# Optimization experiments

Hardware: AMD Instinct MI355X
Metric: run time of the kernel (lower is better)

The kernel has to match this reference:

```python
import jax, jax.numpy as jnp
import numpy as np

EMBED_DIM = 1024
NUM_HEADS = 8
HEAD_DIM = EMBED_DIM // NUM_HEADS  # 128
MAX_DIST = 128
RADIUS = 256
R = 2 * MAX_DIST + 1  # 257 relative-position embeddings


def setup_inputs() -> dict:
    key = jax.random.key(0)
    ks = jax.random.split(key, 8)
    B, Sq, Sk = 4, 1024, 1024
    s = 0.02
    return {
        "Q": jax.random.normal(ks[0], (B, Sq, EMBED_DIM), jnp.float32),
        "K": jax.random.normal(ks[1], (B, Sk, EMBED_DIM), jnp.float32),
        "V": jax.random.normal(ks[2], (B, Sk, EMBED_DIM), jnp.float32),
        "segment_ids": jnp.zeros((B, Sq), jnp.int32),
        "key_padding_mask": jnp.zeros((B, Sk), jnp.bool_),
        "Wq": jax.random.normal(ks[3], (EMBED_DIM, EMBED_DIM), jnp.float32) * s,
        "Wk": jax.random.normal(ks[4], (EMBED_DIM, EMBED_DIM), jnp.float32) * s,
        "Wv": jax.random.normal(ks[5], (EMBED_DIM, EMBED_DIM), jnp.float32) * s,
        "Wo": jax.random.normal(ks[6], (EMBED_DIM, EMBED_DIM), jnp.float32) * s,
        "rel_emb": jax.random.normal(ks[7], (NUM_HEADS, R, HEAD_DIM), jnp.float32) * s,
    }


def _proj(x, W, B, S):
    # Linear (no bias) then split heads: (B,S,d) -> (B*h, S, head_dim)
    y = x @ W.T
    return y.reshape(B, S, NUM_HEADS, HEAD_DIM).transpose(0, 2, 1, 3).reshape(B * NUM_HEADS, S, HEAD_DIM)


def _attention(Q, K, V, key_padding_mask, Wq, Wk, Wv, Wo, rel_emb):
    B, Sq, _ = Q.shape
    Sk = K.shape[1]
    Qp = _proj(Q, Wq, B, Sq)
    Kp = _proj(K, Wk, B, Sk)
    Vp = _proj(V, Wv, B, Sk)

    iq = jnp.arange(Sq)
    ik = jnp.arange(Sk)
    # clipped relative offsets -> bias table indices, shape (Sq, Sk)
    rel_ids = jnp.clip(ik[None, :] - iq[:, None], -MAX_DIST, MAX_DIST) + MAX_DIST

    # per-head table tiled over batch: (B*h, R, head_dim)
    rel_embeds = jnp.broadcast_to(rel_emb[None], (B, NUM_HEADS, R, HEAD_DIM)).reshape(B * NUM_HEADS, R, HEAD_DIM)

    Q_rel = jnp.einsum('bqd,brd->bqr', Qp, rel_embeds)        # (B*h, Sq, R)
    energy = jnp.einsum('bqd,bkd->bqk', Qp, Kp)               # (B*h, Sq, Sk)
    rel_shift = Q_rel[:, iq[:, None], rel_ids]                # gather along R -> (B*h, Sq, Sk)
    energy = (energy + rel_shift) / jnp.sqrt(jnp.float32(HEAD_DIM))

    local_mask = jnp.abs(ik[None, :] - iq[:, None]) > RADIUS  # (Sq, Sk) slided band
    mask = local_mask[None, None] | key_padding_mask[:, None, None, :]  # (B,1,Sq,Sk)
    mask = jnp.broadcast_to(mask, (B, NUM_HEADS, Sq, Sk)).reshape(B * NUM_HEADS, Sq, Sk)
    energy = jnp.where(mask, -jnp.inf, energy)

    attn = jax.nn.softmax(energy, axis=2)
    out = jnp.matmul(attn, Vp)                                # (B*h, Sq, head_dim)
    # permute(0,2,3,1): head_dim-major then head, matching the torch module
    out = out.reshape(B, NUM_HEADS, Sq, HEAD_DIM).transpose(0, 2, 3, 1).reshape(B, Sq, HEAD_DIM * NUM_HEADS)
    return out @ Wo.T


def reference(Q, K, V, segment_ids, key_padding_mask, Wq, Wk, Wv, Wo, rel_emb):
    # segment_ids is unused by the 'slided' RPE variant
    return _attention(Q, K, V, key_padding_mask, Wq, Wk, Wv, Wo, rel_emb)
```

## Files before the change

### kernel.cpp

```cpp
#include <hip/hip_runtime.h>

typedef __attribute__((ext_vector_type(8))) short short8;
typedef __attribute__((ext_vector_type(4))) short short4v;
typedef __attribute__((ext_vector_type(4))) float float4a;
typedef __attribute__((ext_vector_type(16))) float float16a;
typedef __attribute__((ext_vector_type(4))) unsigned int uint4v;

#define MFMA16(a, b, c) __builtin_amdgcn_mfma_f32_16x16x32_bf16(a, b, c, 0, 0, 0)
#define MFMA32(a, b, c) __builtin_amdgcn_mfma_f32_32x32x16_bf16(a, b, c, 0, 0, 0)

static __device__ __forceinline__ short f2bf(float f) {
  unsigned u = __builtin_bit_cast(unsigned, f);
  u += 0x7fff + ((u >> 16) & 1);
  return (short)(u >> 16);
}
static __device__ __forceinline__ float bf2f(short s) {
  unsigned u = ((unsigned)(unsigned short)s) << 16;
  return __builtin_bit_cast(float, u);
}

static __device__ __forceinline__ void gl2lds(const short* g, short* l) {
  __builtin_amdgcn_global_load_lds(
      (const __attribute__((address_space(1))) void*)g,
      (__attribute__((address_space(3))) void*)l,
      16, 0, 0);
}

struct Cvt8 { const float* in[8]; short* out[8]; };
__global__ __launch_bounds__(256) void cvt8_k(Cvt8 a) {
  int b = blockIdx.x, seg, rb;
  if (b < 12288)      { seg = b >> 12;                 rb = b & 4095; }
  else if (b < 16384) { seg = 3 + ((b - 12288) >> 10); rb = (b - 12288) & 1023; }
  else                { seg = 7;                       rb = b - 16384; }
  int i = rb * 256 + threadIdx.x;
  if (seg == 6) {
    int o = i * 4;
    int n = o >> 10, kp = o & 1023;
    int h = kp >> 7, d0 = kp & 127;
    const float* src = a.in[6] + n * 1024 + h;
    short4v s;
    s.x = f2bf(src[d0 * 8]);
    s.y = f2bf(src[d0 * 8 + 8]);
    s.z = f2bf(src[d0 * 8 + 16]);
    s.w = f2bf(src[d0 * 8 + 24]);
    ((short4v*)a.out[6])[i] = s;
    return;
  }
  float4a v = ((const float4a*)a.in[seg])[i];
  short4v o;
  o.x = f2bf(v.x); o.y = f2bf(v.y); o.z = f2bf(v.z); o.w = f2bf(v.w);
  ((short4v*)a.out[seg])[i] = o;
}

__global__ __launch_bounds__(256) void gemm_qkv(
    const short* __restrict__ Qb, const short* __restrict__ Kb, const short* __restrict__ Vb,
    const short* __restrict__ Wq, const short* __restrict__ Wk, const short* __restrict__ Wv,
    short* __restrict__ Qp, short* __restrict__ Kp, short* __restrict__ Vt) {
  __shared__ short pool[32768];
  int bid = blockIdx.x;
  int xcd = bid & 7, slot = bid >> 3;
  int seg = slot >> 5, r = slot & 31;
  int mt = ((xcd >> 1) << 3) | (r >> 2);
  int nt = ((xcd & 1) << 2) | (r & 3);
  const short* A = seg == 0 ? Qb : (seg == 1 ? Kb : Vb);
  const short* W = seg == 0 ? Wq : (seg == 1 ? Wk : Wv);
  int m0 = mt * 128, n0 = nt * 128;
  int tid = threadIdx.x;
  int lane = tid & 63, wid = tid >> 6;
  int l15 = lane & 15, quad = lane >> 4;
  int wm = wid & 1, wn = wid >> 1;

  int srow = lane >> 3, sunit = (lane & 7) ^ (lane >> 3);
  const short* gA = A + (m0 + wid * 32 + srow) * 1024 + sunit * 8;
  const short* gB = W + (n0 + wid * 32 + srow) * 1024 + sunit * 8;
  int stoff = (wid * 32) * 64;
  int sw = l15 & 7;

  float4a acc[4][4];
#pragma unroll
  for (int i = 0; i < 4; ++i)
#pragma unroll
    for (int j = 0; j < 4; ++j) acc[i][j] = (float4a){0, 0, 0, 0};

#pragma unroll
  for (int t = 0; t < 4; ++t) {
    gl2lds(gA + t * 8192, pool + stoff + t * 512);
    gl2lds(gB + t * 8192, pool + 8192 + stoff + t * 512);
  }
  __syncthreads();

  int cur = 0;
  for (int kc = 0; kc < 1024; kc += 64) {
    if (kc < 960) {
      short* nxt = pool + ((cur ^ 1) << 14);
#pragma unroll
      for (int t = 0; t < 4; ++t) {
        gl2lds(gA + kc + 64 + t * 8192, nxt + stoff + t * 512);
        gl2lds(gB + kc + 64 + t * 8192, nxt + 8192 + stoff + t * 512);
      }
    }
    const short* As = pool + (cur << 14);
    const short* Bs = As + 8192;
#pragma unroll
    for (int ks = 0; ks < 2; ++ks) {
      short8 af[4], bfr[4];
#pragma unroll
      for (int i = 0; i < 4; ++i)
        af[i] = *(const short8*)&As[(wm * 64 + i * 16 + l15) * 64 +
                                    (((ks * 4 + quad) ^ sw) * 8)];
#pragma unroll
      for (int j = 0; j < 4; ++j)
        bfr[j] = *(const short8*)&Bs[(wn * 64 + j * 16 + l15) * 64 +
                                     (((ks * 4 + quad) ^ sw) * 8)];
#pragma unroll
      for (int i = 0; i < 4; ++i)
#pragma unroll
        for (int j = 0; j < 4; ++j) acc[i][j] = MFMA16(af[i], bfr[j], acc[i][j]);
    }
    __syncthreads();
    cur ^= 1;
  }

  if (seg < 2) {
    float scl = (seg == 0) ? 0.12752745707470575f : 1.0f;
#pragma unroll
    for (int i = 0; i < 4; ++i)
#pragma unroll
      for (int j = 0; j < 4; ++j)
#pragma unroll
        for (int r2 = 0; r2 < 4; ++r2) {
          int m = m0 + wm * 64 + i * 16 + quad * 4 + r2;
          int n = n0 + wn * 64 + j * 16 + l15;
          int bb = m >> 10, s = m & 1023, hh = n >> 7, d = n & 127;
          short v = f2bf(acc[i][j][r2] * scl);
          if (seg == 0) Qp[(((bb * 8 + hh) * 1024) + s) * 128 + d] = v;
          else          Kp[(((bb * 8 + hh) * 1024) + s) * 128 + d] = v;
        }
  } else {
    short* T = pool;
    int b2 = m0 >> 10, s0 = m0 & 1023;
    long vb2 = (long)(b2 * 8 + nt) * 131072;
#pragma unroll
    for (int hd = 0; hd < 2; ++hd) {
      __syncthreads();
      if (wn == hd) {
#pragma unroll
        for (int j = 0; j < 4; ++j)
#pragma unroll
          for (int i = 0; i < 4; ++i)
#pragma unroll
            for (int r2 = 0; r2 < 4; ++r2)
              T[(j * 16 + l15) * 132 + wm * 64 + i * 16 + quad * 4 + r2] =
                  f2bf(acc[i][j][r2]);
      }
      __syncthreads();
#pragma unroll
      for (int rr = 0; rr < 4; ++rr) {
        int d = rr * 16 + (tid >> 4);
        short8 v = *(const short8*)&T[d * 132 + (tid & 15) * 8];
        *(short8*)&Vt[vb2 + (hd * 64 + d) * 1024 + s0 + (tid & 15) * 8] = v;
      }
    }
  }
}

__global__ __launch_bounds__(256) void gemm_o(const short* __restrict__ A,
                                              const short* __restrict__ W,
                                              float* __restrict__ C) {
  __shared__ short pool[24576];
  int bid = blockIdx.x;
  int xcd = bid & 7, slot = bid >> 3;
  int mt = ((xcd >> 1) << 3) | (slot >> 3);
  int nt = ((xcd & 1) << 3) | (slot & 7);
  int m0 = mt * 128, n0 = nt * 64;
  int lane = threadIdx.x & 63, wid = threadIdx.x >> 6;
  int l15 = lane & 15, quad = lane >> 4;
  int wm = wid & 1, wn = wid >> 1;

  int srow = lane >> 3, sunit = (lane & 7) ^ (lane >> 3);
  int bb = m0 >> 10, q0t = m0 & 1023;
  const short* gA = A + bb * 1048576 + (q0t + wid * 32 + srow) * 128 + sunit * 8;
  const short* gB = W + (n0 + wid * 16 + srow) * 1024 + sunit * 8;
  int saoff = (wid * 32) * 64;
  int sboff = (wid * 16) * 64;
  int sw = l15 & 7;

  float4a acc[4][2];
#pragma unroll
  for (int i = 0; i < 4; ++i)
#pragma unroll
    for (int j = 0; j < 2; ++j) acc[i][j] = (float4a){0, 0, 0, 0};

#pragma unroll
  for (int t = 0; t < 4; ++t) gl2lds(gA + t * 1024, pool + saoff + t * 512);
#pragma unroll
  for (int t = 0; t < 2; ++t) gl2lds(gB + t * 8192, pool + 8192 + sboff + t * 512);
  __syncthreads();

  int cur = 0;
  for (int kc = 0; kc < 1024; kc += 64) {
    if (kc < 960) {
      int kn = kc + 64;
      int koff = (kn >> 7) * 131072 + (kn & 64);
      short* nxt = pool + ((cur ^ 1) * 12288);
#pragma unroll
      for (int t = 0; t < 4; ++t) gl2lds(gA + koff + t * 1024, nxt + saoff + t * 512);
#pragma unroll
      for (int t = 0; t < 2; ++t) gl2lds(gB + kn + t * 8192, nxt + 8192 + sboff + t * 512);
    }
    const short* As = pool + cur * 12288;
    const short* Bs = As + 8192;
#pragma unroll
    for (int ks = 0; ks < 2; ++ks) {
      short8 af[4], bfr[2];
#pragma unroll
      for (int i = 0; i < 4; ++i)
        af[i] = *(const short8*)&As[(wm * 64 + i * 16 + l15) * 64 +
                                    (((ks * 4 + quad) ^ sw) * 8)];
#pragma unroll
      for (int j = 0; j < 2; ++j)
        bfr[j] = *(const short8*)&Bs[(wn * 32 + j * 16 + l15) * 64 +
                                     (((ks * 4 + quad) ^ sw) * 8)];
#pragma unroll
      for (int i = 0; i < 4; ++i)
#pragma unroll
        for (int j = 0; j < 2; ++j) acc[i][j] = MFMA16(af[i], bfr[j], acc[i][j]);
    }
    __syncthreads();
    cur ^= 1;
  }

#pragma unroll
  for (int i = 0; i < 4; ++i)
#pragma unroll
    for (int j = 0; j < 2; ++j)
#pragma unroll
      for (int r2 = 0; r2 < 4; ++r2) {
        int m = m0 + wm * 64 + i * 16 + quad * 4 + r2;
        int n = n0 + wn * 32 + j * 16 + l15;
        C[m * 1024 + n] = acc[i][j][r2];
      }
}

__global__ __launch_bounds__(256) void qrel_k(const short* __restrict__ Qp,
                                              const short* __restrict__ rel,
                                              short* __restrict__ Qrel) {
  int lane = threadIdx.x & 63, wid = threadIdx.x >> 6;
  int gw = blockIdx.x * 4 + wid;
  int bh = gw / 1088;
  int rem = gw - bh * 1088;
  int mt = rem / 17;
  int nt = rem - mt * 17;
  int l15 = lane & 15, quad = lane >> 4;
  int h = bh & 7;

  const short* arow = Qp + bh * 131072 + (mt * 16 + l15) * 128 + quad * 8;
  int col = nt * 16 + l15;
  int colc = col > 256 ? 256 : col;
  const short* brow = rel + (h * 257 + colc) * 128 + quad * 8;

  float4a acc = {0, 0, 0, 0};
#pragma unroll
  for (int kc = 0; kc < 128; kc += 32) {
    short8 a = *(const short8*)(arow + kc);
    short8 b = *(const short8*)(brow + kc);
    acc = MFMA16(a, b, acc);
  }
  if (col < 257) {
#pragma unroll
    for (int r = 0; r < 4; ++r) {
      int q = mt * 16 + quad * 4 + r;
      Qrel[bh * 264192 + q * 258 + col] = f2bf(acc[r]);
    }
  }
}

__global__ __launch_bounds__(256, 2) void attn_k(const short* __restrict__ Qp,
                                                 const short* __restrict__ Kp,
                                                 const short* __restrict__ Vt,
                                                 const short* __restrict__ Qrel,
                                                 const unsigned char* __restrict__ kpm,
                                                 short* __restrict__ O2) {
  __shared__ __align__(16) short pool[16512];
  short* qlds = pool;
  float* obuf = (float*)pool;
  float* lbuf = (float*)pool + 8192;
  int tid = threadIdx.x;
  int lane = tid & 63, wid = tid >> 6;
  int qt = wid & 1, half = wid >> 1;
  int bid = blockIdx.x;
  int bh = ((bid & 7) << 2) | ((bid >> 3) & 3);
  int qsb = bid >> 5;
  int Q0 = qsb * 64;
  int q0 = Q0 + qt * 32;
  int l31 = lane & 31, hl = lane >> 5;
  int b = bh >> 3;

  {
    const short8* src = (const short8*)(Qrel + bh * 264192 + Q0 * 258);
    short8* dst = (short8*)qlds;
    for (int i = tid; i < 2064; i += 256) dst[i] = src[i];
  }

  short8 aq[8];
  const short* qrow = Qp + bh * 131072 + (q0 + l31) * 128 + hl * 8;
#pragma unroll
  for (int s = 0; s < 8; ++s) aq[s] = *(const short8*)(qrow + s * 16);
  __syncthreads();

  float16a O[4];
#pragma unroll
  for (int d = 0; d < 4; ++d)
#pragma unroll
    for (int i = 0; i < 16; ++i) O[d][i] = 0.f;
  float lsum = 0.f;

  int klo = Q0 - 256; if (klo < 0) klo = 0;
  int khi = Q0 + 320; if (khi > 1024) khi = 1024;

  const short* kbase = Kp + bh * 131072 + hl * 8;
  const short* vbase = Vt + bh * 131072 + hl * 8;
  const unsigned char* pmrow = kpm + b * 1024;
  int qv = q0 + l31;
  int rowb = (qt * 32 + l31) * 258;

  int k0 = klo + half * 32;
  short8 kb[8];
  unsigned pm32 = 0;
  {
    const short* krow = kbase + (k0 + l31) * 128;
#pragma unroll
    for (int s = 0; s < 8; ++s) kb[s] = *(const short8*)(krow + s * 16);
    pm32 = (unsigned)__ballot(pmrow[k0 + l31] != 0);
  }

  for (; k0 < khi; k0 += 64) {
    unsigned pmc = pm32;
    float16a S;
#pragma unroll
    for (int i = 0; i < 16; ++i) S[i] = 0.f;
#pragma unroll
    for (int s = 0; s < 8; ++s) S = MFMA32(kb[s], aq[s], S);

    int kn = k0 + 64;
    unsigned char pmb = 0;
    if (kn < khi) {
      const short* krow = kbase + (kn + l31) * 128;
#pragma unroll
      for (int s = 0; s < 8; ++s) kb[s] = *(const short8*)(krow + s * 16);
      pmb = pmrow[kn + l31];
    }

    short8 vb0[4], vb1[4];
#pragma unroll
    for (int dblk = 0; dblk < 4; ++dblk) {
      const short* vrow = vbase + (dblk * 32 + l31) * 1024 + k0;
      vb0[dblk] = *(const short8*)(vrow);
      vb1[dblk] = *(const short8*)(vrow + 16);
    }

    int dq = k0 - qv;
    bool edge = (k0 - q0 < -224) | (k0 - q0 > 224) | (pmc != 0);
    if (!edge) {
      int rb = dq + 4 * hl + 128;
#pragma unroll
      for (int i = 0; i < 16; ++i) {
        int rr = rb + (i & 3) + 8 * (i >> 2);
        rr = rr < 0 ? 0 : (rr > 256 ? 256 : rr);
        float pe = __builtin_amdgcn_exp2f(S[i] + bf2f(qlds[rowb + rr]));
        S[i] = pe;
        lsum += pe;
      }
    } else {
#pragma unroll
      for (int i = 0; i < 16; ++i) {
        int koff = (i & 3) + 8 * (i >> 2) + 4 * hl;
        int dd = dq + koff;
        int rr = dd < -128 ? 0 : (dd > 128 ? 256 : dd + 128);
        float rel = bf2f(qlds[rowb + rr]);
        int msk = (dd < -256) | (dd > 256) | (int)((pmc >> koff) & 1u);
        float pe = msk ? 0.f : __builtin_amdgcn_exp2f(S[i] + rel);
        S[i] = pe;
        lsum += pe;
      }
    }

    short8 ap0, ap1;
    {
      unsigned x0, y0, z0, w0;
      asm("v_cvt_pk_bf16_f32 %0, %1, %2" : "=v"(x0) : "v"(S[0]), "v"(S[1]));
      asm("v_cvt_pk_bf16_f32 %0, %1, %2" : "=v"(y0) : "v"(S[2]), "v"(S[3]));
      asm("v_cvt_pk_bf16_f32 %0, %1, %2" : "=v"(z0) : "v"(S[4]), "v"(S[5]));
      asm("v_cvt_pk_bf16_f32 %0, %1, %2" : "=v"(w0) : "v"(S[6]), "v"(S[7]));
      asm("v_permlane32_swap_b32 %0, %1" : "+v"(x0), "+v"(z0));
      asm("v_permlane32_swap_b32 %0, %1" : "+v"(y0), "+v"(w0));
      uint4v u0 = {x0, y0, z0, w0};
      ap0 = __builtin_bit_cast(short8, u0);
      unsigned x1, y1, z1, w1;
      asm("v_cvt_pk_bf16_f32 %0, %1, %2" : "=v"(x1) : "v"(S[8]), "v"(S[9]));
      asm("v_cvt_pk_bf16_f32 %0, %1, %2" : "=v"(y1) : "v"(S[10]), "v"(S[11]));
      asm("v_cvt_pk_bf16_f32 %0, %1, %2" : "=v"(z1) : "v"(S[12]), "v"(S[13]));
      asm("v_cvt_pk_bf16_f32 %0, %1, %2" : "=v"(w1) : "v"(S[14]), "v"(S[15]));
      asm("v_permlane32_swap_b32 %0, %1" : "+v"(x1), "+v"(z1));
      asm("v_permlane32_swap_b32 %0, %1" : "+v"(y1), "+v"(w1));
      uint4v u1 = {x1, y1, z1, w1};
      ap1 = __builtin_bit_cast(short8, u1);
    }

#pragma unroll
    for (int dblk = 0; dblk < 4; ++dblk) {
      O[dblk] = MFMA32(ap0, vb0[dblk], O[dblk]);
      O[dblk] = MFMA32(ap1, vb1[dblk], O[dblk]);
    }

    pm32 = (unsigned)__ballot(pmb != 0);
  }

  lsum += __shfl_xor(lsum, 32);
  __syncthreads();
  if (half == 1) {
    if (hl == 0) lbuf[qt * 32 + l31] = lsum;
#pragma unroll
    for (int dblk = 0; dblk < 4; ++dblk)
#pragma unroll
      for (int i = 0; i < 16; ++i) {
        int qoff = (i & 3) + 8 * (i >> 2) + 4 * hl;
        obuf[(qt * 32 + qoff) * 128 + dblk * 32 + l31] = O[dblk][i];
      }
  }
  __syncthreads();
  if (half == 0) {
    if (hl == 0) {
      float inv = __builtin_amdgcn_rcpf(lsum + lbuf[qt * 32 + l31]);
      lbuf[qt * 32 + l31] = inv;
    }
#pragma unroll
    for (int dblk = 0; dblk < 4; ++dblk)
#pragma unroll
      for (int i = 0; i < 16; ++i) {
        int qoff = (i & 3) + 8 * (i >> 2) + 4 * hl;
        obuf[(qt * 32 + qoff) * 128 + dblk * 32 + l31] += O[dblk][i];
      }
  }
  __syncthreads();

#pragma unroll
  for (int it = 0; it < 4; ++it) {
    int idx = tid + it * 256;
    int q = idx >> 4, d = (idx & 15) * 8;
    float inv = lbuf[q];
    const float* ob = &obuf[q * 128 + d];
    short8 v;
#pragma unroll
    for (int j = 0; j < 8; ++j) v[j] = f2bf(ob[j] * inv);
    *(short8*)&O2[(long)bh * 131072 + (long)(Q0 + q) * 128 + d] = v;
  }
}

extern "C" void kernel_launch(void* const* d_in, const int* in_sizes, int n_in,
                              void* d_out, int out_size, void* d_ws, size_t ws_size,
                              hipStream_t stream) {
  const float* Q   = (const float*)d_in[0];
  const float* K   = (const float*)d_in[1];
  const float* V   = (const float*)d_in[2];
  const unsigned char* kpm = (const unsigned char*)d_in[4];
  const float* Wq  = (const float*)d_in[5];
  const float* Wk  = (const float*)d_in[6];
  const float* Wv  = (const float*)d_in[7];
  const float* Wo  = (const float*)d_in[8];
  const float* rel = (const float*)d_in[9];
  float* out = (float*)d_out;

  short* ws = (short*)d_ws;
  short* Qb   = ws;
  short* Kb   = Qb + 4194304;
  short* Vb   = Kb + 4194304;
  short* Wqb  = Vb + 4194304;
  short* Wkb  = Wqb + 1048576;
  short* Wvb  = Wkb + 1048576;
  short* Wob  = Wvb + 1048576;
  short* relb = Wob + 1048576;
  short* Qp   = relb + 263168;
  short* Kp   = Qp + 4194304;
  short* Vt   = Kp + 4194304;
  short* O2   = Vt + 4194304;
  short* Qrel = Qb;

  Cvt8 ca;
  ca.in[0] = Q;  ca.out[0] = Qb;
  ca.in[1] = K;  ca.out[1] = Kb;
  ca.in[2] = V;  ca.out[2] = Vb;
  ca.in[3] = Wq; ca.out[3] = Wqb;
  ca.in[4] = Wk; ca.out[4] = Wkb;
  ca.in[5] = Wv; ca.out[5] = Wvb;
  ca.in[6] = Wo; ca.out[6] = Wob;
  ca.in[7] = rel; ca.out[7] = relb;
  cvt8_k<<<dim3(16641), dim3(256), 0, stream>>>(ca);

  gemm_qkv<<<dim3(768), dim3(256), 0, stream>>>(Qb, Kb, Vb, Wqb, Wkb, Wvb, Qp, Kp, Vt);
  qrel_k<<<dim3(8704), dim3(256), 0, stream>>>(Qp, relb, Qrel);
  attn_k<<<dim3(512), dim3(256), 0, stream>>>(Qp, Kp, Vt, Qrel, kpm, O2);
  gemm_o<<<dim3(512), dim3(256), 0, stream>>>(O2, Wob, out);
}
```

Measured before the change: 239.7 us.

## Stage K/V tiles through LDS with async global_load_lds and swizzled layout

Replaces per-wave direct global loads of K and V fragments with cooperative block-level staging into shared memory via global_load_lds, using XOR-swizzled layouts to avoid bank conflicts. Each 64-key tile is loaded once per block and shared by both query-tile waves, which removes the duplicate global traffic between the two waves that previously read the same keys. The cost is doubled LDS allocation, which may reduce occupancy, and two block-wide barriers per iteration. The prefetch of the next tile is issued after the first barrier and overlaps the current tile's compute.

```diff
diff --git a/kernel.cpp b/kernel.cpp
--- a/kernel.cpp
+++ b/kernel.cpp
@@ -281,13 +281,15 @@
                                                  const short* __restrict__ Qrel,
                                                  const unsigned char* __restrict__ kpm,
                                                  short* __restrict__ O2) {
-  __shared__ __align__(16) short pool[16512];
+  __shared__ __align__(16) short pool[32896];
   short* qlds = pool;
-  float* obuf = (float*)pool;
-  float* lbuf = (float*)pool + 8192;
+  short* Kbuf = pool + 16512;
+  short* Vbuf = pool + 16512 + 8192;
+  float* obuf = (float*)(pool + 16512);
+  float* lbuf = (float*)pool;
   int tid = threadIdx.x;
   int lane = tid & 63, wid = tid >> 6;
-  int qt = wid & 1, half = wid >> 1;
+  int qt = wid & 1, kh = wid >> 1;
   int bid = blockIdx.x;
   int bh = ((bid & 7) << 2) | ((bid >> 3) & 3);
   int qsb = bid >> 5;
@@ -296,17 +298,46 @@
   int l31 = lane & 31, hl = lane >> 5;
   int b = bh >> 3;
 
+  int klo = Q0 - 256; if (klo < 0) klo = 0;
+  int khi = Q0 + 320; if (khi > 1024) khi = 1024;
+
+  const short* kgbase = Kp + (long)bh * 131072;
+  const short* vgbase = Vt + (long)bh * 131072;
+  const unsigned char* pmrow = kpm + b * 1024;
+
+  int ksr = lane >> 4, ksu = lane & 15;
+  int vsr = lane >> 3, vsu = (lane & 7) ^ (lane >> 3);
+
+#define STAGE_KV(KT)                                                          \
+  {                                                                           \
+    int _k0 = (KT);                                                           \
+    _Pragma("unroll")                                                         \
+    for (int c = 0; c < 4; ++c) {                                             \
+      int rl = wid * 16 + c * 4 + ksr;                                        \
+      gl2lds(kgbase + (long)(_k0 + rl) * 128 + ((ksu ^ (c * 4 + ksr)) * 8),   \
+             Kbuf + (wid * 16 + c * 4) * 128);                                \
+    }                                                                         \
+    _Pragma("unroll")                                                         \
+    for (int c = 0; c < 4; ++c) {                                             \
+      int rl = wid * 32 + c * 8 + vsr;                                        \
+      gl2lds(vgbase + (long)rl * 1024 + _k0 + vsu * 8,                        \
+             Vbuf + (wid * 32 + c * 8) * 64);                                 \
+    }                                                                         \
+  }
+
   {
     const short8* src = (const short8*)(Qrel + bh * 264192 + Q0 * 258);
     short8* dst = (short8*)qlds;
     for (int i = tid; i < 2064; i += 256) dst[i] = src[i];
   }
-
   short8 aq[8];
   const short* qrow = Qp + bh * 131072 + (q0 + l31) * 128 + hl * 8;
 #pragma unroll
   for (int s = 0; s < 8; ++s) aq[s] = *(const short8*)(qrow + s * 16);
+  STAGE_KV(klo);
+  unsigned char pmb = pmrow[klo + kh * 32 + l31];
   __syncthreads();
+  unsigned pm32 = (unsigned)__ballot(pmb != 0);
 
   float16a O[4];
 #pragma unroll
@@ -315,52 +346,43 @@
     for (int i = 0; i < 16; ++i) O[d][i] = 0.f;
   float lsum = 0.f;
 
-  int klo = Q0 - 256; if (klo < 0) klo = 0;
-  int khi = Q0 + 320; if (khi > 1024) khi = 1024;
-
-  const short* kbase = Kp + bh * 131072 + hl * 8;
-  const short* vbase = Vt + bh * 131072 + hl * 8;
-  const unsigned char* pmrow = kpm + b * 1024;
   int qv = q0 + l31;
   int rowb = (qt * 32 + l31) * 258;
-
-  int k0 = klo + half * 32;
-  short8 kb[8];
-  unsigned pm32 = 0;
-  {
-    const short* krow = kbase + (k0 + l31) * 128;
-#pragma unroll
-    for (int s = 0; s < 8; ++s) kb[s] = *(const short8*)(krow + s * 16);
-    pm32 = (unsigned)__ballot(pmrow[k0 + l31] != 0);
-  }
-
-  for (; k0 < khi; k0 += 64) {
+  int r15 = l31 & 15;
+  int d7 = l31 & 7;
+
+  for (int k0 = klo; k0 < khi; k0 += 64) {
+    int kw = k0 + kh * 32;
+    short8 kf[8];
+    const short* Kr = Kbuf + (kh * 32 + l31) * 128;
+#pragma unroll
+    for (int s = 0; s < 8; ++s)
+      kf[s] = *(const short8*)&Kr[(((2 * s + hl) ^ r15) * 8)];
+    short8 vf0[4], vf1[4];
+#pragma unroll
+    for (int dblk = 0; dblk < 4; ++dblk) {
+      const short* Vr = Vbuf + (dblk * 32 + l31) * 64;
+      vf0[dblk] = *(const short8*)&Vr[(((kh * 4 + hl) ^ d7) * 8)];
+      vf1[dblk] = *(const short8*)&Vr[(((kh * 4 + 2 + hl) ^ d7) * 8)];
+    }
+    __syncthreads();
+
+    int k1 = k0 + 64;
+    unsigned char pmn = 0;
+    if (k1 < khi) {
+      STAGE_KV(k1);
+      pmn = pmrow[k1 + kh * 32 + l31];
+    }
     unsigned pmc = pm32;
+
     float16a S;
 #pragma unroll
     for (int i = 0; i < 16; ++i) S[i] = 0.f;
 #pragma unroll
-    for (int s = 0; s < 8; ++s) S = MFMA32(kb[s], aq[s], S);
-
-    int kn = k0 + 64;
-    unsigned char pmb = 0;
-    if (kn < khi) {
-      const short* krow = kbase + (kn + l31) * 128;
-#pragma unroll
-      for (int s = 0; s < 8; ++s) kb[s] = *(const short8*)(krow + s * 16);
-      pmb = pmrow[kn + l31];
-    }
-
-    short8 vb0[4], vb1[4];
-#pragma unroll
-    for (int dblk = 0; dblk < 4; ++dblk) {
-      const short* vrow = vbase + (dblk * 32 + l31) * 1024 + k0;
-      vb0[dblk] = *(const short8*)(vrow);
-      vb1[dblk] = *(const short8*)(vrow + 16);
-    }
-
-    int dq = k0 - qv;
-    bool edge = (k0 - q0 < -224) | (k0 - q0 > 224) | (pmc != 0);
+    for (int s = 0; s < 8; ++s) S = MFMA32(kf[s], aq[s], S);
+
+    int dq = kw - qv;
+    bool edge = (kw - q0 < -224) | (kw - q0 > 224) | (pmc != 0);
     if (!edge) {
       int rb = dq + 4 * hl + 128;
 #pragma unroll
@@ -409,16 +431,18 @@
 
 #pragma unroll
     for (int dblk = 0; dblk < 4; ++dblk) {
-      O[dblk] = MFMA32(ap0, vb0[dblk], O[dblk]);
-      O[dblk] = MFMA32(ap1, vb1[dblk], O[dblk]);
-    }
-
-    pm32 = (unsigned)__ballot(pmb != 0);
-  }
+      O[dblk] = MFMA32(ap0, vf0[dblk], O[dblk]);
+      O[dblk] = MFMA32(ap1, vf1[dblk], O[dblk]);
+    }
+
+    __syncthreads();
+    pm32 = (unsigned)__ballot(pmn != 0);
+  }
+#undef STAGE_KV
 
   lsum += __shfl_xor(lsum, 32);
   __syncthreads();
-  if (half == 1) {
+  if (kh == 1) {
     if (hl == 0) lbuf[qt * 32 + l31] = lsum;
 #pragma unroll
     for (int dblk = 0; dblk < 4; ++dblk)
@@ -429,7 +453,7 @@
       }
   }
   __syncthreads();
-  if (half == 0) {
+  if (kh == 0) {
     if (hl == 0) {
       float inv = __builtin_amdgcn_rcpf(lsum + lbuf[qt * 32 + l31]);
       lbuf[qt * 32 + l31] = inv;
```

Result: faster. 220.5 us (-8.0%).
